# Optimization experiments

Hardware: AMD Instinct MI355X
Metric: run time of the kernel (lower is better)

## Reference

```python
import jax, jax.numpy as jnp
import numpy as np

N_HEAD = 16


def setup_inputs() -> dict:
    key = jax.random.key(0)
    ks = jax.random.split(key, 7)
    b, lq, lv = 2, 2048, 2048
    q_dim = k_dim = v_dim = 1024
    s = 0.02
    return {
        "q": jax.random.normal(ks[0], (b, lq, q_dim), jnp.float32),
        "k": jax.random.normal(ks[1], (b, lv, k_dim), jnp.float32),
        "v": jax.random.normal(ks[2], (b, lv, v_dim), jnp.float32),
        "Wq": jax.random.normal(ks[3], (k_dim, q_dim), jnp.float32) * s,  # torch Linear: [out, in]
        "Wk": jax.random.normal(ks[4], (k_dim, k_dim), jnp.float32) * s,
        "Wv": jax.random.normal(ks[5], (v_dim, v_dim), jnp.float32) * s,
        "Wo": jax.random.normal(ks[6], (v_dim, v_dim), jnp.float32) * s,
    }


def reference(q, k, v, Wq, Wk, Wv, Wo):
    b, lq, _ = q.shape
    lv = k.shape[1]
    qp = q @ Wq.T  # [b, lq, k_dim]
    kp = k @ Wk.T  # [b, lv, k_dim]
    vp = v @ Wv.T  # [b, lv, v_dim]
    # split heads: [b, h, l, d]
    qh = qp.reshape(b, lq, N_HEAD, -1).transpose(0, 2, 1, 3)
    kh = kp.reshape(b, lv, N_HEAD, -1).transpose(0, 2, 1, 3)
    vh = vp.reshape(b, lv, N_HEAD, -1).transpose(0, 2, 1, 3)
    d = qh.shape[-1]
    scores = jnp.einsum("bhqd,bhkd->bhqk", qh, kh) / jnp.sqrt(jnp.float32(d))
    p = jax.nn.softmax(scores, axis=-1)
    attn = jnp.einsum("bhqk,bhkd->bhqd", p, vh)
    attn = attn.transpose(0, 2, 1, 3).reshape(b, lq, -1)  # [b, lq, v_dim]
    return attn @ Wo.T
```

## Files before the change

kernel.cpp:

```cpp
#include <hip/hip_runtime.h>
#include <hip/hip_bf16.h>
#include <stdint.h>

typedef __attribute__((ext_vector_type(8))) short bf16x8;
typedef __attribute__((ext_vector_type(4))) float f32x4;
typedef __attribute__((ext_vector_type(16))) float f32x16;
typedef __attribute__((ext_vector_type(2))) uint32_t u32x2;
typedef __attribute__((ext_vector_type(4))) uint32_t u32x4;

#define LQ 2048
#define CDIM 1024
#define NTOK 4096
#define WELEM 1048576
#define TELEM 4194304

__device__ __forceinline__ short f2bf(float f) {
  union { float f; uint32_t u; } v; v.f = f;
  uint32_t r = v.u + 0x7fffu + ((v.u >> 16) & 1u);
  return (short)(r >> 16);
}

__device__ __forceinline__ uint32_t cvt_pk_bf16(float a, float b) {
  uint32_t r;
  asm("v_cvt_pk_bf16_f32 %0, %1, %2" : "=v"(r) : "v"(a), "v"(b));
  return r;
}

__device__ __forceinline__ int swz(int row, int col) {
  return (row << 6) + (col ^ ((row & 7) << 3));
}

__device__ __forceinline__ void gl_lds16(const void* g, void* lds) {
  __builtin_amdgcn_global_load_lds(
      (const __attribute__((address_space(1))) void*)g,
      (__attribute__((address_space(3))) void*)lds, 16, 0, 0);
}

__device__ __forceinline__ void plswap(uint32_t& a, uint32_t& b) {
  asm volatile("s_nop 1\n\tv_permlane32_swap_b32 %0, %1\n\ts_nop 1" : "+v"(a), "+v"(b));
}

__device__ __forceinline__ bf16x8 mkfrag(const float* p) {
  uint32_t w0 = cvt_pk_bf16(p[0], p[1]);
  uint32_t w1 = cvt_pk_bf16(p[2], p[3]);
  uint32_t w2 = cvt_pk_bf16(p[4], p[5]);
  uint32_t w3 = cvt_pk_bf16(p[6], p[7]);
  plswap(w0, w2);
  plswap(w1, w3);
  union { u32x4 u; bf16x8 h; } cv;
  cv.u = u32x4{w0, w1, w2, w3};
  return cv.h;
}

__global__ __launch_bounds__(256) void convall_kernel(const float* __restrict__ wq, const float* __restrict__ wk,
                                                      const float* __restrict__ wv, const float* __restrict__ wo,
                                                      const float* __restrict__ q, const float* __restrict__ k,
                                                      const float* __restrict__ v,
                                                      short* __restrict__ wbf, short* __restrict__ qb,
                                                      short* __restrict__ kb, short* __restrict__ vb) {
  const int NG = (4 * WELEM + 3 * TELEM) / 8;
  for (int i = blockIdx.x * 256 + threadIdx.x; i < NG; i += gridDim.x * 256) {
    int e = i * 8;
    const float* s;
    short* d;
    if (e < 4 * WELEM) {
      int seg = e >> 20;
      int off = e & (WELEM - 1);
      s = (seg == 0 ? wq : seg == 1 ? wk : seg == 2 ? wv : wo) + off;
      d = wbf + e;
    } else {
      int j = e - 4 * WELEM;
      int which = j >> 22;
      int off = j & (TELEM - 1);
      s = (which == 0 ? q : which == 1 ? k : v) + off;
      d = (which == 0 ? qb : which == 1 ? kb : vb) + off;
    }
    f32x4 x0 = *(const f32x4*)(s);
    f32x4 x1 = *(const f32x4*)(s + 4);
    u32x4 r = { cvt_pk_bf16(x0[0], x0[1]), cvt_pk_bf16(x0[2], x0[3]),
                cvt_pk_bf16(x1[0], x1[1]), cvt_pk_bf16(x1[2], x1[3]) };
    *(u32x4*)(d) = r;
  }
}

template<bool OUT_BF16, int BN>
__device__ __forceinline__ void gemm_bb(const short* __restrict__ Ap, const short* __restrict__ Bp,
                                        void* Cp, int m0, int n0, int K, int ldc)
{
  __shared__ alignas(16) short Ab[2][128 * 64];
  __shared__ alignas(16) short Bb[2][BN * 64];

  const int t = threadIdx.x;
  const int lane = t & 63;
  const int wid = t >> 6;
  const int l15 = lane & 15, l4 = lane >> 4;
  constexpr int NI = (BN == 128) ? 4 : 2;
  const int wr = (BN == 128) ? (wid >> 1) * 64 : wid * 32;
  const int wc = (BN == 128) ? (wid & 1) * 64 : 0;

  f32x4 acc[NI][4];
#pragma unroll
  for (int i = 0; i < NI; ++i)
#pragma unroll
    for (int j = 0; j < 4; ++j) acc[i][j] = f32x4{0.f, 0.f, 0.f, 0.f};

  const int grow = lane >> 3;
  const int gcol = ((lane & 7) ^ grow) * 8;
  constexpr int AI = 4, BI = BN / 32;
  const short* asrc = Ap + (size_t)(m0 + wid * 32 + grow) * K + gcol;
  const short* bsrc = Bp + (size_t)(n0 + wid * (BN / 4) + grow) * K + gcol;

#pragma unroll
  for (int c = 0; c < AI; ++c) gl_lds16(asrc + (size_t)c * 8 * K, &Ab[0][(wid * AI + c) * 512]);
#pragma unroll
  for (int c = 0; c < BI; ++c) gl_lds16(bsrc + (size_t)c * 8 * K, &Bb[0][(wid * BI + c) * 512]);

  const int NT = K / 64;
  for (int kt = 0; kt < NT; ++kt) {
    const int cur = kt & 1;
    if (kt + 1 < NT) {
      const short* a2 = asrc + (size_t)(kt + 1) * 64;
      const short* b2 = bsrc + (size_t)(kt + 1) * 64;
#pragma unroll
      for (int c = 0; c < AI; ++c) gl_lds16(a2 + (size_t)c * 8 * K, &Ab[cur ^ 1][(wid * AI + c) * 512]);
#pragma unroll
      for (int c = 0; c < BI; ++c) gl_lds16(b2 + (size_t)c * 8 * K, &Bb[cur ^ 1][(wid * BI + c) * 512]);
      if constexpr (BN == 128) asm volatile("s_waitcnt vmcnt(8)" ::: "memory");
      else                     asm volatile("s_waitcnt vmcnt(6)" ::: "memory");
    } else {
      asm volatile("s_waitcnt vmcnt(0)" ::: "memory");
    }
    __builtin_amdgcn_sched_barrier(0);
    __builtin_amdgcn_s_barrier();
    __builtin_amdgcn_sched_barrier(0);

    const short* Al = Ab[cur];
    const short* Bl = Bb[cur];
#pragma unroll
    for (int kh = 0; kh < 2; ++kh) {
      bf16x8 af[NI], bfr[4];
#pragma unroll
      for (int i = 0; i < NI; ++i)
        af[i] = *(const bf16x8*)&Al[swz(wr + i * 16 + l15, kh * 32 + l4 * 8)];
#pragma unroll
      for (int j = 0; j < 4; ++j)
        bfr[j] = *(const bf16x8*)&Bl[swz(wc + j * 16 + l15, kh * 32 + l4 * 8)];
      __builtin_amdgcn_s_setprio(1);
#pragma unroll
      for (int i = 0; i < NI; ++i)
#pragma unroll
        for (int j = 0; j < 4; ++j)
          acc[i][j] = __builtin_amdgcn_mfma_f32_16x16x32_bf16(af[i], bfr[j], acc[i][j], 0, 0, 0);
      __builtin_amdgcn_s_setprio(0);
    }
    __builtin_amdgcn_sched_barrier(0);
    __builtin_amdgcn_s_barrier();
  }

#pragma unroll
  for (int i = 0; i < NI; ++i)
#pragma unroll
    for (int j = 0; j < 4; ++j)
#pragma unroll
      for (int r = 0; r < 4; ++r) {
        int rr = m0 + wr + i * 16 + l4 * 4 + r;
        int cc = n0 + wc + j * 16 + l15;
        if (OUT_BF16) ((short*)Cp)[(size_t)rr * ldc + cc] = f2bf(acc[i][j][r]);
        else          ((float*)Cp)[(size_t)rr * ldc + cc] = acc[i][j][r];
      }
}

__global__ __launch_bounds__(256) void proj_kernel(const short* __restrict__ qb, const short* __restrict__ kb,
                                                   const short* __restrict__ vb, const short* __restrict__ wbf,
                                                   short* __restrict__ qp, short* __restrict__ kp,
                                                   short* __restrict__ vp)
{
  int nb = blockIdx.y;
  int sel = nb >> 3;
  int n0 = (nb & 7) * 128;
  int m0 = blockIdx.x * 128;
  const short* A = sel == 0 ? qb : (sel == 1 ? kb : vb);
  const short* B = wbf + (size_t)sel * WELEM;
  short* C = sel == 0 ? qp : (sel == 1 ? kp : vp);
  gemm_bb<true, 128>(A, B, C, m0, n0, CDIM, CDIM);
}

__global__ __launch_bounds__(256) void out_kernel(const short* __restrict__ at, const short* __restrict__ wo,
                                                  float* __restrict__ out)
{
  gemm_bb<false, 64>(at, wo, out, blockIdx.x * 128, blockIdx.y * 64, CDIM, CDIM);
}

__global__ __launch_bounds__(256) void attn_kernel(const short* __restrict__ kp, const short* __restrict__ vp,
                                                   short* __restrict__ qp)
{
  __shared__ alignas(16) short Kbuf[2][64 * 64];
  __shared__ alignas(16) short Vbuf[2][64 * 64];

  const int bh = blockIdx.x;
  const int b = bh >> 4, h = bh & 15;
  const int q0 = blockIdx.y * 128;
  const int t = threadIdx.x, lane = t & 63, wid = t >> 6;
  const int l31 = lane & 31, hi = lane >> 5;
  const size_t base = (size_t)b * LQ * CDIM + (size_t)h * 64;
  const int qw = q0 + wid * 32;

  bf16x8 qf[4];
  {
    const short* qrow = qp + base + (size_t)(qw + l31) * CDIM + hi * 8;
    qf[0] = *(const bf16x8*)(qrow);
    qf[1] = *(const bf16x8*)(qrow + 16);
    qf[2] = *(const bf16x8*)(qrow + 32);
    qf[3] = *(const bf16x8*)(qrow + 48);
  }

  bf16x8 ones;
#pragma unroll
  for (int j = 0; j < 8; ++j) ones[j] = (short)0x3F80;

  f32x16 o0, o1, lacc;
#pragma unroll
  for (int r = 0; r < 16; ++r) { o0[r] = 0.f; o1[r] = 0.f; lacc[r] = 0.f; }
  float mrun = -1e30f;

  const int krow_in_grp = lane >> 3;
  const int kchunk = (lane & 7) ^ krow_in_grp;
  const short* ksrc0 = kp + base + (size_t)(wid * 16 + krow_in_grp) * CDIM + kchunk * 8;
  const int vd0 = wid * 16;
  const short* vsrc0 = vp + base + (size_t)lane * CDIM + vd0;

  const float SC2 = 0.18033688011112042f;
  const float THR2 = 11.54f;
  const int NT = LQ / 64;

  bf16x8 vv0, vv1;
  gl_lds16(ksrc0, &Kbuf[0][(wid * 16) * 64]);
  gl_lds16(ksrc0 + (size_t)8 * CDIM, &Kbuf[0][(wid * 16 + 8) * 64]);
  vv0 = *(const bf16x8*)(vsrc0);
  vv1 = *(const bf16x8*)(vsrc0 + 8);

  for (int kt = 0; kt < NT; ++kt) {
    const int cur = kt & 1;
    asm volatile("s_waitcnt vmcnt(0)" ::: "memory");
#pragma unroll
    for (int j = 0; j < 8; ++j) Vbuf[cur][swz(vd0 + j, lane)] = vv0[j];
#pragma unroll
    for (int j = 0; j < 8; ++j) Vbuf[cur][swz(vd0 + 8 + j, lane)] = vv1[j];
    __syncthreads();

    if (kt + 1 < NT) {
      const short* ks = ksrc0 + (size_t)(kt + 1) * 64 * CDIM;
      gl_lds16(ks, &Kbuf[cur ^ 1][(wid * 16) * 64]);
      gl_lds16(ks + (size_t)8 * CDIM, &Kbuf[cur ^ 1][(wid * 16 + 8) * 64]);
      const short* vs = vsrc0 + (size_t)(kt + 1) * 64 * CDIM;
      vv0 = *(const bf16x8*)(vs);
      vv1 = *(const bf16x8*)(vs + 8);
    }
    __builtin_amdgcn_sched_barrier(0);

    const short* Klds = Kbuf[cur];
    const short* Vt = Vbuf[cur];
    f32x16 c0, c1;
#pragma unroll
    for (int r = 0; r < 16; ++r) { c0[r] = 0.f; c1[r] = 0.f; }
    __builtin_amdgcn_s_setprio(1);
#pragma unroll
    for (int ds = 0; ds < 4; ++ds) {
      bf16x8 ka = *(const bf16x8*)&Klds[swz(l31, ds * 16 + hi * 8)];
      bf16x8 kb = *(const bf16x8*)&Klds[swz(32 + l31, ds * 16 + hi * 8)];
      c0 = __builtin_amdgcn_mfma_f32_32x32x16_bf16(ka, qf[ds], c0, 0, 0, 0);
      c1 = __builtin_amdgcn_mfma_f32_32x32x16_bf16(kb, qf[ds], c1, 0, 0, 0);
    }
    __builtin_amdgcn_s_setprio(0);

    float m = fmaxf(c0[0], c0[1]);
#pragma unroll
    for (int r = 2; r < 16; r += 2) m = fmaxf(fmaxf(m, c0[r]), c0[r + 1]);
#pragma unroll
    for (int r = 0; r < 16; r += 2) m = fmaxf(fmaxf(m, c1[r]), c1[r + 1]);
    m = fmaxf(m, __shfl_xor(m, 32, 64));
    float mx2 = m * SC2;
    if (__any(mx2 > mrun + THR2)) {
      float mn = fmaxf(mrun, mx2);
      float cr = exp2f(mrun - mn);
      mrun = mn;
      lacc[0] *= cr;
#pragma unroll
      for (int r = 0; r < 16; ++r) { o0[r] *= cr; o1[r] *= cr; }
    }
    float pr0[16], pr1[16];
#pragma unroll
    for (int r = 0; r < 16; ++r) {
      pr0[r] = exp2f(fmaf(c0[r], SC2, -mrun));
      pr1[r] = exp2f(fmaf(c1[r], SC2, -mrun));
    }

    bf16x8 pa0 = mkfrag(pr0);
    bf16x8 pa1 = mkfrag(pr0 + 8);
    bf16x8 pa2 = mkfrag(pr1);
    bf16x8 pa3 = mkfrag(pr1 + 8);

    __builtin_amdgcn_s_setprio(1);
#pragma unroll
    for (int ks = 0; ks < 4; ++ks) {
      bf16x8 pa = ks == 0 ? pa0 : ks == 1 ? pa1 : ks == 2 ? pa2 : pa3;
      bf16x8 v0 = *(const bf16x8*)&Vt[swz(l31, ks * 16 + hi * 8)];
      bf16x8 v1 = *(const bf16x8*)&Vt[swz(32 + l31, ks * 16 + hi * 8)];
      o0 = __builtin_amdgcn_mfma_f32_32x32x16_bf16(v0, pa, o0, 0, 0, 0);
      o1 = __builtin_amdgcn_mfma_f32_32x32x16_bf16(v1, pa, o1, 0, 0, 0);
      lacc = __builtin_amdgcn_mfma_f32_32x32x16_bf16(ones, pa, lacc, 0, 0, 0);
    }
    __builtin_amdgcn_s_setprio(0);
  }

  float inv = 1.0f / lacc[0];
  short* orow = qp + base + (size_t)(qw + l31) * CDIM;
#pragma unroll
  for (int rq = 0; rq < 4; ++rq) {
    u32x2 w;
    w[0] = cvt_pk_bf16(o0[rq * 4 + 0] * inv, o0[rq * 4 + 1] * inv);
    w[1] = cvt_pk_bf16(o0[rq * 4 + 2] * inv, o0[rq * 4 + 3] * inv);
    *(u32x2*)(orow + rq * 8 + hi * 4) = w;
    w[0] = cvt_pk_bf16(o1[rq * 4 + 0] * inv, o1[rq * 4 + 1] * inv);
    w[1] = cvt_pk_bf16(o1[rq * 4 + 2] * inv, o1[rq * 4 + 3] * inv);
    *(u32x2*)(orow + 32 + rq * 8 + hi * 4) = w;
  }
}

extern "C" void kernel_launch(void* const* d_in, const int* in_sizes, int n_in,
                              void* d_out, int out_size, void* d_ws, size_t ws_size,
                              hipStream_t stream) {
  const float* q  = (const float*)d_in[0];
  const float* k  = (const float*)d_in[1];
  const float* v  = (const float*)d_in[2];
  const float* Wq = (const float*)d_in[3];
  const float* Wk = (const float*)d_in[4];
  const float* Wv = (const float*)d_in[5];
  const float* Wo = (const float*)d_in[6];
  float* out = (float*)d_out;

  short* wbf = (short*)d_ws;
  short* vb  = wbf + (size_t)4 * WELEM;
  short* qp  = vb + (size_t)TELEM;
  short* kp  = qp + (size_t)TELEM;
  short* vp  = kp + (size_t)TELEM;
  short* qb = (short*)d_out;
  short* kb = qb + (size_t)TELEM;

  convall_kernel<<<2048, 256, 0, stream>>>(Wq, Wk, Wv, Wo, q, k, v, wbf, qb, kb, vb);
  proj_kernel<<<dim3(32, 24), 256, 0, stream>>>(qb, kb, vb, wbf, qp, kp, vp);
  attn_kernel<<<dim3(32, 16), 256, 0, stream>>>(kp, vp, qp);
  out_kernel<<<dim3(32, 16), 256, 0, stream>>>(qp, wbf + (size_t)3 * WELEM, out);
}
```

Baseline: 142.1 us.

## Write V projection transposed per head and stream it into LDS asynchronously

The V projection epilogue now writes V in a per-(batch,head) transposed layout [bh][d][token]. The attention kernel can then load V tiles into LDS with global_load_lds, just like K, instead of staging them in registers and scattering them with element-wise LDS stores. The pipeline now uses a partial vmcnt wait and explicit barriers, and exp2f is replaced by raw v_exp_f32 with a max reduction split into four chains. The cost moves to scattered 2-byte stores in the projection epilogue, which may be poorly coalesced.

```diff
diff --git a/kernel.cpp b/kernel.cpp
--- a/kernel.cpp
+++ b/kernel.cpp
@@ -23,6 +23,12 @@
 __device__ __forceinline__ uint32_t cvt_pk_bf16(float a, float b) {
   uint32_t r;
   asm("v_cvt_pk_bf16_f32 %0, %1, %2" : "=v"(r) : "v"(a), "v"(b));
+  return r;
+}
+
+__device__ __forceinline__ float fexp2(float x) {
+  float r;
+  asm("v_exp_f32 %0, %1" : "=v"(r) : "v"(x));
   return r;
 }
 
@@ -83,7 +89,7 @@
   }
 }
 
-template<bool OUT_BF16, int BN>
+template<int CMODE, int BN>
 __device__ __forceinline__ void gemm_bb(const short* __restrict__ Ap, const short* __restrict__ Bp,
                                         void* Cp, int m0, int n0, int K, int ldc)
 {
@@ -165,33 +171,43 @@
       for (int r = 0; r < 4; ++r) {
         int rr = m0 + wr + i * 16 + l4 * 4 + r;
         int cc = n0 + wc + j * 16 + l15;
-        if (OUT_BF16) ((short*)Cp)[(size_t)rr * ldc + cc] = f2bf(acc[i][j][r]);
-        else          ((float*)Cp)[(size_t)rr * ldc + cc] = acc[i][j][r];
+        if constexpr (CMODE == 0) {
+          ((float*)Cp)[(size_t)rr * ldc + cc] = acc[i][j][r];
+        } else if constexpr (CMODE == 1) {
+          ((short*)Cp)[(size_t)rr * ldc + cc] = f2bf(acc[i][j][r]);
+        } else {
+          size_t idx = ((size_t)(((rr >> 11) << 4) + (cc >> 6)) * 64 + (cc & 63)) * 2048 + (rr & 2047);
+          ((short*)Cp)[idx] = f2bf(acc[i][j][r]);
+        }
       }
 }
 
 __global__ __launch_bounds__(256) void proj_kernel(const short* __restrict__ qb, const short* __restrict__ kb,
                                                    const short* __restrict__ vb, const short* __restrict__ wbf,
                                                    short* __restrict__ qp, short* __restrict__ kp,
-                                                   short* __restrict__ vp)
+                                                   short* __restrict__ vpt)
 {
   int nb = blockIdx.y;
   int sel = nb >> 3;
   int n0 = (nb & 7) * 128;
   int m0 = blockIdx.x * 128;
-  const short* A = sel == 0 ? qb : (sel == 1 ? kb : vb);
-  const short* B = wbf + (size_t)sel * WELEM;
-  short* C = sel == 0 ? qp : (sel == 1 ? kp : vp);
-  gemm_bb<true, 128>(A, B, C, m0, n0, CDIM, CDIM);
+  if (sel == 2) {
+    gemm_bb<2, 128>(vb, wbf + (size_t)2 * WELEM, vpt, m0, n0, CDIM, CDIM);
+  } else {
+    const short* A = sel == 0 ? qb : kb;
+    const short* B = wbf + (size_t)sel * WELEM;
+    short* C = sel == 0 ? qp : kp;
+    gemm_bb<1, 128>(A, B, C, m0, n0, CDIM, CDIM);
+  }
 }
 
 __global__ __launch_bounds__(256) void out_kernel(const short* __restrict__ at, const short* __restrict__ wo,
                                                   float* __restrict__ out)
 {
-  gemm_bb<false, 64>(at, wo, out, blockIdx.x * 128, blockIdx.y * 64, CDIM, CDIM);
-}
-
-__global__ __launch_bounds__(256) void attn_kernel(const short* __restrict__ kp, const short* __restrict__ vp,
+  gemm_bb<0, 64>(at, wo, out, blockIdx.x * 128, blockIdx.y * 64, CDIM, CDIM);
+}
+
+__global__ __launch_bounds__(256) void attn_kernel(const short* __restrict__ kp, const short* __restrict__ vpt,
                                                    short* __restrict__ qp)
 {
   __shared__ alignas(16) short Kbuf[2][64 * 64];
@@ -223,43 +239,40 @@
   for (int r = 0; r < 16; ++r) { o0[r] = 0.f; o1[r] = 0.f; lacc[r] = 0.f; }
   float mrun = -1e30f;
 
-  const int krow_in_grp = lane >> 3;
-  const int kchunk = (lane & 7) ^ krow_in_grp;
-  const short* ksrc0 = kp + base + (size_t)(wid * 16 + krow_in_grp) * CDIM + kchunk * 8;
-  const int vd0 = wid * 16;
-  const short* vsrc0 = vp + base + (size_t)lane * CDIM + vd0;
+  const int grp = lane >> 3;
+  const int chk = ((lane & 7) ^ grp) * 8;
+  const short* ksrc = kp + base + (size_t)(wid * 16 + grp) * CDIM + chk;
+  const short* vsrc = vpt + (size_t)bh * 64 * 2048 + (size_t)(wid * 16 + grp) * 2048 + chk;
 
   const float SC2 = 0.18033688011112042f;
   const float THR2 = 11.54f;
   const int NT = LQ / 64;
 
-  bf16x8 vv0, vv1;
-  gl_lds16(ksrc0, &Kbuf[0][(wid * 16) * 64]);
-  gl_lds16(ksrc0 + (size_t)8 * CDIM, &Kbuf[0][(wid * 16 + 8) * 64]);
-  vv0 = *(const bf16x8*)(vsrc0);
-  vv1 = *(const bf16x8*)(vsrc0 + 8);
+  gl_lds16(ksrc, &Kbuf[0][(wid * 16) * 64]);
+  gl_lds16(ksrc + (size_t)8 * CDIM, &Kbuf[0][(wid * 16 + 8) * 64]);
+  gl_lds16(vsrc, &Vbuf[0][(wid * 16) * 64]);
+  gl_lds16(vsrc + (size_t)8 * 2048, &Vbuf[0][(wid * 16 + 8) * 64]);
 
   for (int kt = 0; kt < NT; ++kt) {
     const int cur = kt & 1;
-    asm volatile("s_waitcnt vmcnt(0)" ::: "memory");
-#pragma unroll
-    for (int j = 0; j < 8; ++j) Vbuf[cur][swz(vd0 + j, lane)] = vv0[j];
-#pragma unroll
-    for (int j = 0; j < 8; ++j) Vbuf[cur][swz(vd0 + 8 + j, lane)] = vv1[j];
-    __syncthreads();
-
     if (kt + 1 < NT) {
-      const short* ks = ksrc0 + (size_t)(kt + 1) * 64 * CDIM;
+      const short* ks = ksrc + (size_t)(kt + 1) * 64 * CDIM;
+      const short* vs = vsrc + (size_t)(kt + 1) * 64;
       gl_lds16(ks, &Kbuf[cur ^ 1][(wid * 16) * 64]);
       gl_lds16(ks + (size_t)8 * CDIM, &Kbuf[cur ^ 1][(wid * 16 + 8) * 64]);
-      const short* vs = vsrc0 + (size_t)(kt + 1) * 64 * CDIM;
-      vv0 = *(const bf16x8*)(vs);
-      vv1 = *(const bf16x8*)(vs + 8);
-    }
+      gl_lds16(vs, &Vbuf[cur ^ 1][(wid * 16) * 64]);
+      gl_lds16(vs + (size_t)8 * 2048, &Vbuf[cur ^ 1][(wid * 16 + 8) * 64]);
+      asm volatile("s_waitcnt vmcnt(4)" ::: "memory");
+    } else {
+      asm volatile("s_waitcnt vmcnt(0)" ::: "memory");
+    }
+    __builtin_amdgcn_sched_barrier(0);
+    __builtin_amdgcn_s_barrier();
     __builtin_amdgcn_sched_barrier(0);
 
     const short* Klds = Kbuf[cur];
     const short* Vt = Vbuf[cur];
+
     f32x16 c0, c1;
 #pragma unroll
     for (int r = 0; r < 16; ++r) { c0[r] = 0.f; c1[r] = 0.f; }
@@ -273,16 +286,21 @@
     }
     __builtin_amdgcn_s_setprio(0);
 
-    float m = fmaxf(c0[0], c0[1]);
-#pragma unroll
-    for (int r = 2; r < 16; r += 2) m = fmaxf(fmaxf(m, c0[r]), c0[r + 1]);
-#pragma unroll
-    for (int r = 0; r < 16; r += 2) m = fmaxf(fmaxf(m, c1[r]), c1[r + 1]);
+    float ma = fmaxf(c0[0], c1[0]), mb = fmaxf(c0[1], c1[1]);
+    float mc = fmaxf(c0[2], c1[2]), md = fmaxf(c0[3], c1[3]);
+#pragma unroll
+    for (int r = 4; r < 16; r += 4) {
+      ma = fmaxf(ma, fmaxf(c0[r], c1[r]));
+      mb = fmaxf(mb, fmaxf(c0[r + 1], c1[r + 1]));
+      mc = fmaxf(mc, fmaxf(c0[r + 2], c1[r + 2]));
+      md = fmaxf(md, fmaxf(c0[r + 3], c1[r + 3]));
+    }
+    float m = fmaxf(fmaxf(ma, mb), fmaxf(mc, md));
     m = fmaxf(m, __shfl_xor(m, 32, 64));
     float mx2 = m * SC2;
     if (__any(mx2 > mrun + THR2)) {
       float mn = fmaxf(mrun, mx2);
-      float cr = exp2f(mrun - mn);
+      float cr = fexp2(mrun - mn);
       mrun = mn;
       lacc[0] *= cr;
 #pragma unroll
@@ -291,8 +309,8 @@
     float pr0[16], pr1[16];
 #pragma unroll
     for (int r = 0; r < 16; ++r) {
-      pr0[r] = exp2f(fmaf(c0[r], SC2, -mrun));
-      pr1[r] = exp2f(fmaf(c1[r], SC2, -mrun));
+      pr0[r] = fexp2(fmaf(c0[r], SC2, -mrun));
+      pr1[r] = fexp2(fmaf(c1[r], SC2, -mrun));
     }
 
     bf16x8 pa0 = mkfrag(pr0);
@@ -311,6 +329,8 @@
       lacc = __builtin_amdgcn_mfma_f32_32x32x16_bf16(ones, pa, lacc, 0, 0, 0);
     }
     __builtin_amdgcn_s_setprio(0);
+    __builtin_amdgcn_sched_barrier(0);
+    __builtin_amdgcn_s_barrier();
   }
 
   float inv = 1.0f / lacc[0];
@@ -343,12 +363,12 @@
   short* vb  = wbf + (size_t)4 * WELEM;
   short* qp  = vb + (size_t)TELEM;
   short* kp  = qp + (size_t)TELEM;
-  short* vp  = kp + (size_t)TELEM;
+  short* vpt = kp + (size_t)TELEM;
   short* qb = (short*)d_out;
   short* kb = qb + (size_t)TELEM;
 
   convall_kernel<<<2048, 256, 0, stream>>>(Wq, Wk, Wv, Wo, q, k, v, wbf, qb, kb, vb);
-  proj_kernel<<<dim3(32, 24), 256, 0, stream>>>(qb, kb, vb, wbf, qp, kp, vp);
-  attn_kernel<<<dim3(32, 16), 256, 0, stream>>>(kp, vp, qp);
+  proj_kernel<<<dim3(32, 24), 256, 0, stream>>>(qb, kb, vb, wbf, qp, kp, vpt);
+  attn_kernel<<<dim3(32, 16), 256, 0, stream>>>(kp, vpt, qp);
   out_kernel<<<dim3(32, 16), 256, 0, stream>>>(qp, wbf + (size_t)3 * WELEM, out);
 }
```

Measured after the change: 142.7 us. About the same (+0.4%).
